# Kernel optimization log

Hardware: AMD Instinct MI355X
Metric: run time of the kernel (lower is better)

The kernel has to match this reference:

```python
import jax, jax.numpy as jnp
import numpy as np

DIM = 1024
NUM_HEADS = 16
HEAD_DIM = DIM // NUM_HEADS
SCALE = HEAD_DIM ** -0.5


def setup_inputs() -> dict:
    key = jax.random.key(0)
    ks = jax.random.split(key, 5)
    B, N, C = 2, 2048, DIM
    x = jax.random.normal(ks[0], (B, N, C), dtype=jnp.float32)
    s = 1.0 / np.sqrt(C)
    W_qkv = jax.random.normal(ks[1], (C, 3 * C), dtype=jnp.float32) * s
    b_qkv = jax.random.normal(ks[2], (3 * C,), dtype=jnp.float32) * 0.01
    W_proj = jax.random.normal(ks[3], (C, C), dtype=jnp.float32) * s
    b_proj = jax.random.normal(ks[4], (C,), dtype=jnp.float32) * 0.01
    return {"x": x, "W_qkv": W_qkv, "b_qkv": b_qkv, "W_proj": W_proj, "b_proj": b_proj}


def reference(x, W_qkv, b_qkv, W_proj, b_proj):
    B, N, C = x.shape
    qkv = x @ W_qkv + b_qkv                      # [B, N, 3C]
    qkv = qkv.reshape(B, N, 3, NUM_HEADS, HEAD_DIM)
    qkv = jnp.transpose(qkv, (2, 0, 3, 1, 4))    # [3, B, H, N, hd]
    # Faithful to source quirk: q = k = v = qkv[2]
    v = qkv[2]
    q = v
    k = v
    attn = jnp.einsum('bhnd,bhmd->bhnm', q, k) * SCALE
    attn = jax.nn.softmax(attn, axis=-1)
    out = jnp.einsum('bhnm,bhmd->bhnd', attn, v)  # [B, H, N, hd]
    out = jnp.transpose(out, (0, 2, 1, 3)).reshape(B, N, C)
    return out @ W_proj + b_proj
```

## Files before the change

### kernel.cpp

```cpp
#include <hip/hip_runtime.h>

typedef __bf16    bf16x4 __attribute__((ext_vector_type(4)));
typedef __bf16    bf16x8 __attribute__((ext_vector_type(8)));
typedef _Float16  f16x2  __attribute__((ext_vector_type(2)));
typedef _Float16  f16x4  __attribute__((ext_vector_type(4)));
typedef _Float16  f16x8  __attribute__((ext_vector_type(8)));
typedef float     f32x4  __attribute__((ext_vector_type(4)));

#define MFMA16x16x32 __builtin_amdgcn_mfma_f32_16x16x32_bf16
#define MFMA16x16x32F __builtin_amdgcn_mfma_f32_16x16x32_f16

__device__ __forceinline__ void gload_lds16(const void* g, void* l) {
  __builtin_amdgcn_global_load_lds((const __attribute__((address_space(1))) void*)g,
                                   (__attribute__((address_space(3))) void*)l, 16, 0, 0);
}

__device__ __forceinline__ f16x2 pkrtz(float a, float b) {
  return __builtin_bit_cast(f16x2, __builtin_amdgcn_cvt_pkrtz(a, b));
}

__global__ __launch_bounds__(256) void prep_all(const float* __restrict__ x,
                                                const float* __restrict__ Wqkv,
                                                const float* __restrict__ Wproj,
                                                __bf16* __restrict__ xb,
                                                __bf16* __restrict__ WvT,
                                                __bf16* __restrict__ WpT) {
  __shared__ float tile[64][65];
  const int t = threadIdx.x;
  if (blockIdx.z == 2) {
    const int bid = blockIdx.x * 16 + blockIdx.y;
#pragma unroll
    for (int c = 0; c < 16; c++) {
      int gid = (bid * 16 + c) * 256 + t;
      float4 v = ((const float4*)x)[gid];
      bf16x4 o;
      o.x = (__bf16)v.x; o.y = (__bf16)v.y; o.z = (__bf16)v.z; o.w = (__bf16)v.w;
      *(bf16x4*)&xb[(size_t)gid * 4] = o;
    }
    return;
  }
  const float* src; __bf16* dst; int ld, c0;
  if (blockIdx.z == 0) { src = Wqkv; dst = WvT; ld = 3072; c0 = 2048; }
  else                 { src = Wproj; dst = WpT; ld = 1024; c0 = 0; }
  const int k0 = blockIdx.x * 64, n0 = blockIdx.y * 64;
#pragma unroll
  for (int i = 0; i < 4; i++) {
    int idx = t + i * 256; int r = idx >> 4, g = idx & 15;
    float4 v = *(const float4*)&src[(size_t)(k0 + r) * ld + c0 + n0 + g * 4];
    tile[r][g * 4 + 0] = v.x; tile[r][g * 4 + 1] = v.y;
    tile[r][g * 4 + 2] = v.z; tile[r][g * 4 + 3] = v.w;
  }
  __syncthreads();
#pragma unroll
  for (int i = 0; i < 4; i++) {
    int idx = t + i * 256; int n = idx >> 4, g = idx & 15;
    bf16x4 o;
    o.x = (__bf16)tile[g * 4 + 0][n]; o.y = (__bf16)tile[g * 4 + 1][n];
    o.z = (__bf16)tile[g * 4 + 2][n]; o.w = (__bf16)tile[g * 4 + 3][n];
    *(bf16x4*)&dst[(size_t)(n0 + n) * 1024 + k0 + g * 4] = o;
  }
}

#define STAGE_TILE(bi, kk)                                            \
  { char* buf_ = (char*)lds + (bi) * 24576;                           \
    const __bf16* a_ = pA + (kk) * 64;                                \
    const __bf16* b_ = pB + (kk) * 64;                                \
    gload_lds16(a_,          buf_ + t * 16);                          \
    gload_lds16(a_ + 32 * K, buf_ + 4096  + t * 16);                  \
    gload_lds16(a_ + 64 * K, buf_ + 8192  + t * 16);                  \
    gload_lds16(a_ + 96 * K, buf_ + 12288 + t * 16);                  \
    gload_lds16(b_,          buf_ + 16384 + t * 16);                  \
    gload_lds16(b_ + 32 * K, buf_ + 20480 + t * 16); }

__global__ __launch_bounds__(256, 2) void gemm_v(const __bf16* __restrict__ xb,
                                                 const __bf16* __restrict__ WvT,
                                                 const float* __restrict__ bias,
                                                 __bf16* __restrict__ V,
                                                 _Float16* __restrict__ Vt) {
  constexpr int K = 1024;
  __shared__ char lds[3 * 24576];
  const int t = threadIdx.x, w = t >> 6, l = t & 63, lr = l & 15, quad = l >> 4;
  const int wr = w >> 1, wc = w & 1;
  const int wgid = blockIdx.x;
  const int xcd = wgid & 7, sub = wgid >> 3;
  const int mb = xcd * 4 + (sub & 3), nb = sub >> 2;
  const int m0 = mb * 128, n0 = nb * 64;

  const int row0 = t >> 3;
  const int scol = (t & 7) ^ (row0 & 7);
  const __bf16* pA = xb  + (size_t)(m0 + row0) * K + scol * 8;
  const __bf16* pB = WvT + (size_t)(n0 + row0) * K + scol * 8;

  f32x4 acc[4][2] = {};
  int aoff[4][2], boff[2][2];
#pragma unroll
  for (int mi = 0; mi < 4; mi++)
#pragma unroll
    for (int ks = 0; ks < 2; ks++)
      aoff[mi][ks] = (wr * 64 + mi * 16 + lr) * 128 + (((ks * 4 + quad) ^ (lr & 7)) * 16);
#pragma unroll
  for (int nc = 0; nc < 2; nc++)
#pragma unroll
    for (int ks = 0; ks < 2; ks++)
      boff[nc][ks] = 16384 + (wc * 32 + nc * 16 + lr) * 128 + (((ks * 4 + quad) ^ (lr & 7)) * 16);

  STAGE_TILE(0, 0);
  STAGE_TILE(1, 1);
  for (int it = 0; it < 16; ++it) {
    if (it < 15) { asm volatile("s_waitcnt vmcnt(6)" ::: "memory"); }
    else         { asm volatile("s_waitcnt vmcnt(0)" ::: "memory"); }
    __builtin_amdgcn_sched_barrier(0);
    __builtin_amdgcn_s_barrier();
    if (it + 2 < 16) STAGE_TILE((it + 2) % 3, it + 2);
    const char* buf = (const char*)lds + (it % 3) * 24576;
    bf16x8 af[4][2], bv[2][2];
#pragma unroll
    for (int mi = 0; mi < 4; mi++)
#pragma unroll
      for (int ks = 0; ks < 2; ks++)
        af[mi][ks] = *(const bf16x8*)(buf + aoff[mi][ks]);
#pragma unroll
    for (int nc = 0; nc < 2; nc++)
#pragma unroll
      for (int ks = 0; ks < 2; ks++)
        bv[nc][ks] = *(const bf16x8*)(buf + boff[nc][ks]);
#pragma unroll
    for (int mi = 0; mi < 4; mi++)
#pragma unroll
      for (int nc = 0; nc < 2; nc++)
#pragma unroll
        for (int ks = 0; ks < 2; ks++)
          acc[mi][nc] = MFMA16x16x32(af[mi][ks], bv[nc][ks], acc[mi][nc], 0, 0, 0);
  }
  __syncthreads();
  char* tbuf = (char*)lds;
#pragma unroll
  for (int mi = 0; mi < 4; mi++) {
    const int grow0 = m0 + wr * 64 + mi * 16 + quad * 4;
    const int tokl = wr * 64 + mi * 16 + quad * 4;
#pragma unroll
    for (int nc = 0; nc < 2; nc++) {
      const int d = wc * 32 + nc * 16 + lr;
      const int gcol = n0 + d;
      float bb = bias[gcol];
      float v0 = acc[mi][nc][0] + bb, v1 = acc[mi][nc][1] + bb;
      float v2 = acc[mi][nc][2] + bb, v3 = acc[mi][nc][3] + bb;
      V[(size_t)(grow0 + 0) * 1024 + gcol] = (__bf16)v0;
      V[(size_t)(grow0 + 1) * 1024 + gcol] = (__bf16)v1;
      V[(size_t)(grow0 + 2) * 1024 + gcol] = (__bf16)v2;
      V[(size_t)(grow0 + 3) * 1024 + gcol] = (__bf16)v3;
      f16x2 lo = pkrtz(v0, v1), hi = pkrtz(v2, v3);
      f16x4 pv; pv[0] = lo[0]; pv[1] = lo[1]; pv[2] = hi[0]; pv[3] = hi[1];
      const int g = (tokl >> 2) ^ ((d & 7) << 2);
      *(f16x4*)(tbuf + d * 256 + g * 8) = pv;
    }
  }
  __syncthreads();
  {
    const int b_ = m0 >> 11, tok0 = m0 & 2047;
    const int d = t >> 2, c = t & 3;
    _Float16* dst = Vt + ((size_t)(b_ * 16 + nb) * 64 + d) * 2048 + tok0 + c * 32;
#pragma unroll
    for (int p2 = 0; p2 < 4; p2++) {
      int g = (c * 8 + p2 * 2) ^ ((d & 7) << 2);
      f16x8 vv = *(const f16x8*)(tbuf + d * 256 + g * 8);
      *(f16x8*)&dst[p2 * 8] = vv;
    }
  }
}

__global__ __launch_bounds__(256, 2) void gemm_proj(const __bf16* __restrict__ A,
                                                    const __bf16* __restrict__ Bt,
                                                    const float* __restrict__ bias,
                                                    float* __restrict__ outp) {
  constexpr int K = 1024, Nn = 1024;
  __shared__ char lds[3 * 24576];
  const int t = threadIdx.x, w = t >> 6, l = t & 63, lr = l & 15, quad = l >> 4;
  const int wr = w >> 1, wc = w & 1;
  const int wgid = blockIdx.x;
  const int xcd = wgid & 7, sub = wgid >> 3;
  const int mb = xcd * 4 + (sub & 3), nb = sub >> 2;
  const int m0 = mb * 128, n0 = nb * 64;

  const int row0 = t >> 3;
  const int scol = (t & 7) ^ (row0 & 7);
  const __bf16* pA = A  + (size_t)(m0 + row0) * K + scol * 8;
  const __bf16* pB = Bt + (size_t)(n0 + row0) * K + scol * 8;

  f32x4 acc[4][2] = {};
  int aoff[4][2], boff[2][2];
#pragma unroll
  for (int mi = 0; mi < 4; mi++)
#pragma unroll
    for (int ks = 0; ks < 2; ks++)
      aoff[mi][ks] = (wr * 64 + mi * 16 + lr) * 128 + (((ks * 4 + quad) ^ (lr & 7)) * 16);
#pragma unroll
  for (int nc = 0; nc < 2; nc++)
#pragma unroll
    for (int ks = 0; ks < 2; ks++)
      boff[nc][ks] = 16384 + (wc * 32 + nc * 16 + lr) * 128 + (((ks * 4 + quad) ^ (lr & 7)) * 16);

  STAGE_TILE(0, 0);
  STAGE_TILE(1, 1);
  for (int it = 0; it < 16; ++it) {
    if (it < 15) { asm volatile("s_waitcnt vmcnt(6)" ::: "memory"); }
    else         { asm volatile("s_waitcnt vmcnt(0)" ::: "memory"); }
    __builtin_amdgcn_sched_barrier(0);
    __builtin_amdgcn_s_barrier();
    if (it + 2 < 16) STAGE_TILE((it + 2) % 3, it + 2);
    const char* buf = (const char*)lds + (it % 3) * 24576;
    bf16x8 af[4][2], bv[2][2];
#pragma unroll
    for (int mi = 0; mi < 4; mi++)
#pragma unroll
      for (int ks = 0; ks < 2; ks++)
        af[mi][ks] = *(const bf16x8*)(buf + aoff[mi][ks]);
#pragma unroll
    for (int nc = 0; nc < 2; nc++)
#pragma unroll
      for (int ks = 0; ks < 2; ks++)
        bv[nc][ks] = *(const bf16x8*)(buf + boff[nc][ks]);
#pragma unroll
    for (int mi = 0; mi < 4; mi++)
#pragma unroll
      for (int nc = 0; nc < 2; nc++)
#pragma unroll
        for (int ks = 0; ks < 2; ks++)
          acc[mi][nc] = MFMA16x16x32(af[mi][ks], bv[nc][ks], acc[mi][nc], 0, 0, 0);
  }
#pragma unroll
  for (int mi = 0; mi < 4; mi++) {
    const int grow0 = m0 + wr * 64 + mi * 16 + quad * 4;
#pragma unroll
    for (int nc = 0; nc < 2; nc++) {
      const int gcol = n0 + wc * 32 + nc * 16 + lr;
      float bb = bias[gcol];
#pragma unroll
      for (int r = 0; r < 4; r++)
        outp[(size_t)(grow0 + r) * Nn + gcol] = acc[mi][nc][r] + bb;
    }
  }
}

__global__ __launch_bounds__(512, 4) void attn_kernel(const __bf16* __restrict__ V,
                                                      const _Float16* __restrict__ Vt,
                                                      __bf16* __restrict__ O) {
  __shared__ char lds[65536];
  const int t = threadIdx.x, w = t >> 6, l = t & 63, lr = l & 15, quad = l >> 4;
  const int bh = blockIdx.x, b = bh >> 4, h = bh & 15;
  const int qb = blockIdx.y * 128 + (w & 3) * 16;
  const int part = w >> 2;

  const __bf16* Vbh = V + (size_t)b * 2048 * 1024 + h * 64;
  const _Float16* Vtbh = Vt + (size_t)bh * 64 * 2048;

  bf16x8 qf[2][2];
#pragma unroll
  for (int sub = 0; sub < 2; sub++)
#pragma unroll
    for (int ks = 0; ks < 2; ks++)
      qf[sub][ks] = *(const bf16x8*)(Vbh + (size_t)(qb + sub * 64 + lr) * 1024 + ks * 32 + quad * 8);

  const int kva = t >> 3, ua = (t & 7) ^ (kva & 7);
  const __bf16* pK0 = Vbh + (size_t)kva * 1024 + ua * 8;
  const __bf16* pK1 = pK0 + (size_t)64 * 1024;
  const int kb_ = t >> 7, d_ = (t >> 1) & 63, qh = (t & 1) ^ ((d_ >> 2) & 1);
  const _Float16* pV0 = Vtbh + (size_t)d_ * 2048 + kb_ * 16 + qh * 8;
  const _Float16* pV1 = pV0 + 64;

  const int koff0 = lr * 128 + ((quad ^ (lr & 7)) * 16);
  const int koff1 = lr * 128 + (((4 + quad) ^ (lr & 7)) * 16);
  const int xq = (quad >> 1) ^ ((lr >> 2) & 1);
  const int voff = lr * 32 + xq * 16 + (quad & 1) * 8;

  f32x4 o[2][4] = {};
  f32x4 l5[2] = {};
  f16x8 ones8;
#pragma unroll
  for (int i = 0; i < 8; i++) ones8[i] = (_Float16)1.0f;
  const float Cc = 0.18033688011112042f;
  const float C8 = 11.541560327111707f;

  {
    char* base = lds;
    gload_lds16(pK0, base + t * 16);
    gload_lds16(pV0, base + 8192 + t * 16);
    gload_lds16(pK1, base + 16384 + t * 16);
    gload_lds16(pV1, base + 24576 + t * 16);
  }
  for (int it = 0; it < 16; ++it) {
    __syncthreads();
    if (it + 1 < 16) {
      pK0 += 131072; pK1 += 131072; pV0 += 128; pV1 += 128;
      char* base = lds + ((it + 1) & 1) * 32768;
      gload_lds16(pK0, base + t * 16);
      gload_lds16(pV0, base + 8192 + t * 16);
      gload_lds16(pK1, base + 16384 + t * 16);
      gload_lds16(pV1, base + 24576 + t * 16);
    }
    const char* Kb = lds + (it & 1) * 32768 + part * 16384;
    const char* Vb = Kb + 8192;

    f32x4 s[2][4] = {};
#pragma unroll
    for (int ks = 0; ks < 2; ks++) {
      const int ko = ks ? koff1 : koff0;
#pragma unroll
      for (int rb = 0; rb < 4; rb++) {
        bf16x8 kf = *(const bf16x8*)(Kb + ko + rb * 2048);
        s[0][rb] = MFMA16x16x32(kf, qf[0][ks], s[0][rb], 0, 0, 0);
        s[1][rb] = MFMA16x16x32(kf, qf[1][ks], s[1][rb], 0, 0, 0);
      }
    }

    f16x8 pf8[2][2];
#pragma unroll
    for (int sub = 0; sub < 2; sub++)
#pragma unroll
      for (int i = 0; i < 2; i++) {
        f16x4 half_[2];
#pragma unroll
        for (int hh = 0; hh < 2; hh++) {
          const int rb = 2 * i + hh;
          float p0 = __builtin_amdgcn_exp2f(s[sub][rb][0] * Cc - C8);
          float p1 = __builtin_amdgcn_exp2f(s[sub][rb][1] * Cc - C8);
          float p2 = __builtin_amdgcn_exp2f(s[sub][rb][2] * Cc - C8);
          float p3 = __builtin_amdgcn_exp2f(s[sub][rb][3] * Cc - C8);
          f16x2 lo = pkrtz(p0, p1);
          f16x2 hi = pkrtz(p2, p3);
          half_[hh][0] = lo[0]; half_[hh][1] = lo[1];
          half_[hh][2] = hi[0]; half_[hh][3] = hi[1];
        }
        pf8[sub][i] = __builtin_shufflevector(half_[0], half_[1], 0, 1, 2, 3, 4, 5, 6, 7);
      }

#pragma unroll
    for (int i = 0; i < 2; i++) {
#pragma unroll
      for (int db = 0; db < 4; db++) {
        f16x4 va = *(const f16x4*)(Vb + voff + db * 512 + (2 * i) * 2048);
        f16x4 vb2 = *(const f16x4*)(Vb + voff + db * 512 + (2 * i + 1) * 2048);
        f16x8 vf8 = __builtin_shufflevector(va, vb2, 0, 1, 2, 3, 4, 5, 6, 7);
        o[0][db] = MFMA16x16x32F(pf8[0][i], vf8, o[0][db], 0, 0, 0);
        o[1][db] = MFMA16x16x32F(pf8[1][i], vf8, o[1][db], 0, 0, 0);
      }
      l5[0] = MFMA16x16x32F(pf8[0][i], ones8, l5[0], 0, 0, 0);
      l5[1] = MFMA16x16x32F(pf8[1][i], ones8, l5[1], 0, 0, 0);
    }
  }

  __syncthreads();
  float* xch = (float*)lds;
  if (w >= 4) {
    float* dsto = xch + (w - 4) * 2048;
#pragma unroll
    for (int sub = 0; sub < 2; sub++)
#pragma unroll
      for (int db = 0; db < 4; db++)
        *(f32x4*)&dsto[(sub * 4 + db) * 256 + l * 4] = o[sub][db];
    float* dstl = xch + 8192 + (w - 4) * 512;
    *(f32x4*)&dstl[l * 4] = l5[0];
    *(f32x4*)&dstl[256 + l * 4] = l5[1];
  }
  __syncthreads();
  if (w < 4) {
    const float* srco = xch + w * 2048;
    const float* srcl = xch + 8192 + w * 512;
#pragma unroll
    for (int sub = 0; sub < 2; sub++) {
#pragma unroll
      for (int db = 0; db < 4; db++)
        o[sub][db] += *(const f32x4*)&srco[(sub * 4 + db) * 256 + l * 4];
      l5[sub] += *(const f32x4*)&srcl[sub * 256 + l * 4];
    }
#pragma unroll
    for (int sub = 0; sub < 2; sub++)
#pragma unroll
      for (int r = 0; r < 4; r++) {
        float lv = 1.0f / l5[sub][r];
        int token = b * 2048 + qb + sub * 64 + quad * 4 + r;
#pragma unroll
        for (int db = 0; db < 4; db++)
          O[(size_t)token * 1024 + h * 64 + db * 16 + lr] = (__bf16)(o[sub][db][r] * lv);
      }
  }
}

extern "C" void kernel_launch(void* const* d_in, const int* in_sizes, int n_in,
                              void* d_out, int out_size, void* d_ws, size_t ws_size,
                              hipStream_t stream) {
  (void)in_sizes; (void)n_in; (void)out_size; (void)ws_size;
  const float* x     = (const float*)d_in[0];
  const float* Wqkv  = (const float*)d_in[1];
  const float* bqkv  = (const float*)d_in[2];
  const float* Wproj = (const float*)d_in[3];
  const float* bproj = (const float*)d_in[4];

  char* ws = (char*)d_ws;
  __bf16*    V   = (__bf16*)(ws);
  _Float16*  Vt  = (_Float16*)(ws + (size_t)8  * 1048576);
  __bf16*    Ob  = (__bf16*)(ws + (size_t)16 * 1048576);
  __bf16*    xb  = (__bf16*)(ws + (size_t)16 * 1048576);
  __bf16*    WvT = (__bf16*)(ws + (size_t)24 * 1048576);
  __bf16*    WpT = (__bf16*)(ws + (size_t)26 * 1048576);

  prep_all<<<dim3(16, 16, 3), 256, 0, stream>>>(x, Wqkv, Wproj, xb, WvT, WpT);
  gemm_v<<<dim3(512), 256, 0, stream>>>(xb, WvT, bqkv + 2048, V, Vt);
  attn_kernel<<<dim3(32, 16), 512, 0, stream>>>(V, Vt, Ob);
  gemm_proj<<<dim3(512), 256, 0, stream>>>(Ob, WpT, bproj, (float*)d_out);
}
```

Measured before the change: 156.8 us.

## Enlarge GEMM tiles to 128x128 with K=32 steps and direct Vt stores

Both GEMMs move from 128x64 output tiles with K=64 stages to 128x128 tiles with K=32 stages, halving the grid to 256 workgroups (one per CU) and raising arithmetic intensity per LDS load. gemm_v also drops the LDS transpose staging for Vt and writes f16x4 strips directly to global memory. The trade-off is lower occupancy (one workgroup per CU), twice as many pipeline iterations with barriers, and less coalesced Vt stores.

```diff
diff --git a/kernel.cpp b/kernel.cpp
--- a/kernel.cpp
+++ b/kernel.cpp
@@ -61,87 +61,72 @@
   }
 }
 
-#define STAGE_TILE(bi, kk)                                            \
-  { char* buf_ = (char*)lds + (bi) * 24576;                           \
-    const __bf16* a_ = pA + (kk) * 64;                                \
-    const __bf16* b_ = pB + (kk) * 64;                                \
+#define STAGE_TILE32(bi, kk)                                          \
+  { char* buf_ = (char*)lds + (bi) * 16384;                           \
+    const __bf16* a_ = pA + (kk) * 32;                                \
+    const __bf16* b_ = pB + (kk) * 32;                                \
     gload_lds16(a_,          buf_ + t * 16);                          \
-    gload_lds16(a_ + 32 * K, buf_ + 4096  + t * 16);                  \
-    gload_lds16(a_ + 64 * K, buf_ + 8192  + t * 16);                  \
-    gload_lds16(a_ + 96 * K, buf_ + 12288 + t * 16);                  \
-    gload_lds16(b_,          buf_ + 16384 + t * 16);                  \
-    gload_lds16(b_ + 32 * K, buf_ + 20480 + t * 16); }
-
-__global__ __launch_bounds__(256, 2) void gemm_v(const __bf16* __restrict__ xb,
+    gload_lds16(a_ + 64 * K, buf_ + 4096  + t * 16);                  \
+    gload_lds16(b_,          buf_ + 8192  + t * 16);                  \
+    gload_lds16(b_ + 64 * K, buf_ + 12288 + t * 16); }
+
+__global__ __launch_bounds__(256, 1) void gemm_v(const __bf16* __restrict__ xb,
                                                  const __bf16* __restrict__ WvT,
                                                  const float* __restrict__ bias,
                                                  __bf16* __restrict__ V,
                                                  _Float16* __restrict__ Vt) {
   constexpr int K = 1024;
-  __shared__ char lds[3 * 24576];
+  __shared__ char lds[3 * 16384];
   const int t = threadIdx.x, w = t >> 6, l = t & 63, lr = l & 15, quad = l >> 4;
   const int wr = w >> 1, wc = w & 1;
   const int wgid = blockIdx.x;
   const int xcd = wgid & 7, sub = wgid >> 3;
   const int mb = xcd * 4 + (sub & 3), nb = sub >> 2;
-  const int m0 = mb * 128, n0 = nb * 64;
-
-  const int row0 = t >> 3;
-  const int scol = (t & 7) ^ (row0 & 7);
+  const int m0 = mb * 128, n0 = nb * 128;
+
+  const int row0 = t >> 2;
+  const int scol = (t & 3) ^ (row0 & 3);
   const __bf16* pA = xb  + (size_t)(m0 + row0) * K + scol * 8;
   const __bf16* pB = WvT + (size_t)(n0 + row0) * K + scol * 8;
 
-  f32x4 acc[4][2] = {};
-  int aoff[4][2], boff[2][2];
+  f32x4 acc[4][4] = {};
+  int aoff[4], boff[4];
 #pragma unroll
   for (int mi = 0; mi < 4; mi++)
-#pragma unroll
-    for (int ks = 0; ks < 2; ks++)
-      aoff[mi][ks] = (wr * 64 + mi * 16 + lr) * 128 + (((ks * 4 + quad) ^ (lr & 7)) * 16);
-#pragma unroll
-  for (int nc = 0; nc < 2; nc++)
-#pragma unroll
-    for (int ks = 0; ks < 2; ks++)
-      boff[nc][ks] = 16384 + (wc * 32 + nc * 16 + lr) * 128 + (((ks * 4 + quad) ^ (lr & 7)) * 16);
-
-  STAGE_TILE(0, 0);
-  STAGE_TILE(1, 1);
-  for (int it = 0; it < 16; ++it) {
-    if (it < 15) { asm volatile("s_waitcnt vmcnt(6)" ::: "memory"); }
+    aoff[mi] = (wr * 64 + mi * 16 + lr) * 64 + ((quad ^ (lr & 3)) * 16);
+#pragma unroll
+  for (int nc = 0; nc < 4; nc++)
+    boff[nc] = 8192 + (wc * 64 + nc * 16 + lr) * 64 + ((quad ^ (lr & 3)) * 16);
+
+  STAGE_TILE32(0, 0);
+  STAGE_TILE32(1, 1);
+  for (int it = 0; it < 32; ++it) {
+    if (it < 31) { asm volatile("s_waitcnt vmcnt(4)" ::: "memory"); }
     else         { asm volatile("s_waitcnt vmcnt(0)" ::: "memory"); }
     __builtin_amdgcn_sched_barrier(0);
     __builtin_amdgcn_s_barrier();
-    if (it + 2 < 16) STAGE_TILE((it + 2) % 3, it + 2);
-    const char* buf = (const char*)lds + (it % 3) * 24576;
-    bf16x8 af[4][2], bv[2][2];
+    if (it + 2 < 32) STAGE_TILE32((it + 2) % 3, it + 2);
+    const char* buf = (const char*)lds + (it % 3) * 16384;
+    bf16x8 af[4], bv[4];
+#pragma unroll
+    for (int mi = 0; mi < 4; mi++) af[mi] = *(const bf16x8*)(buf + aoff[mi]);
+#pragma unroll
+    for (int nc = 0; nc < 4; nc++) bv[nc] = *(const bf16x8*)(buf + boff[nc]);
 #pragma unroll
     for (int mi = 0; mi < 4; mi++)
 #pragma unroll
-      for (int ks = 0; ks < 2; ks++)
-        af[mi][ks] = *(const bf16x8*)(buf + aoff[mi][ks]);
-#pragma unroll
-    for (int nc = 0; nc < 2; nc++)
-#pragma unroll
-      for (int ks = 0; ks < 2; ks++)
-        bv[nc][ks] = *(const bf16x8*)(buf + boff[nc][ks]);
-#pragma unroll
-    for (int mi = 0; mi < 4; mi++)
-#pragma unroll
-      for (int nc = 0; nc < 2; nc++)
-#pragma unroll
-        for (int ks = 0; ks < 2; ks++)
-          acc[mi][nc] = MFMA16x16x32(af[mi][ks], bv[nc][ks], acc[mi][nc], 0, 0, 0);
-  }
-  __syncthreads();
-  char* tbuf = (char*)lds;
+      for (int nc = 0; nc < 4; nc++)
+        acc[mi][nc] = MFMA16x16x32(af[mi], bv[nc], acc[mi][nc], 0, 0, 0);
+  }
+  const int h2 = nb * 2 + wc;
 #pragma unroll
   for (int mi = 0; mi < 4; mi++) {
     const int grow0 = m0 + wr * 64 + mi * 16 + quad * 4;
-    const int tokl = wr * 64 + mi * 16 + quad * 4;
-#pragma unroll
-    for (int nc = 0; nc < 2; nc++) {
-      const int d = wc * 32 + nc * 16 + lr;
-      const int gcol = n0 + d;
+    const int b_ = grow0 >> 11, tok0 = grow0 & 2047;
+#pragma unroll
+    for (int nc = 0; nc < 4; nc++) {
+      const int d2 = nc * 16 + lr;
+      const int gcol = n0 + wc * 64 + d2;
       float bb = bias[gcol];
       float v0 = acc[mi][nc][0] + bb, v1 = acc[mi][nc][1] + bb;
       float v2 = acc[mi][nc][2] + bb, v3 = acc[mi][nc][3] + bb;
@@ -151,89 +136,64 @@
       V[(size_t)(grow0 + 3) * 1024 + gcol] = (__bf16)v3;
       f16x2 lo = pkrtz(v0, v1), hi = pkrtz(v2, v3);
       f16x4 pv; pv[0] = lo[0]; pv[1] = lo[1]; pv[2] = hi[0]; pv[3] = hi[1];
-      const int g = (tokl >> 2) ^ ((d & 7) << 2);
-      *(f16x4*)(tbuf + d * 256 + g * 8) = pv;
-    }
-  }
-  __syncthreads();
-  {
-    const int b_ = m0 >> 11, tok0 = m0 & 2047;
-    const int d = t >> 2, c = t & 3;
-    _Float16* dst = Vt + ((size_t)(b_ * 16 + nb) * 64 + d) * 2048 + tok0 + c * 32;
-#pragma unroll
-    for (int p2 = 0; p2 < 4; p2++) {
-      int g = (c * 8 + p2 * 2) ^ ((d & 7) << 2);
-      f16x8 vv = *(const f16x8*)(tbuf + d * 256 + g * 8);
-      *(f16x8*)&dst[p2 * 8] = vv;
-    }
-  }
-}
-
-__global__ __launch_bounds__(256, 2) void gemm_proj(const __bf16* __restrict__ A,
+      *(f16x4*)&Vt[((size_t)(b_ * 16 + h2) * 64 + d2) * 2048 + tok0] = pv;
+    }
+  }
+}
+
+__global__ __launch_bounds__(256, 1) void gemm_proj(const __bf16* __restrict__ A,
                                                     const __bf16* __restrict__ Bt,
                                                     const float* __restrict__ bias,
                                                     float* __restrict__ outp) {
   constexpr int K = 1024, Nn = 1024;
-  __shared__ char lds[3 * 24576];
+  __shared__ char lds[3 * 16384];
   const int t = threadIdx.x, w = t >> 6, l = t & 63, lr = l & 15, quad = l >> 4;
   const int wr = w >> 1, wc = w & 1;
   const int wgid = blockIdx.x;
   const int xcd = wgid & 7, sub = wgid >> 3;
   const int mb = xcd * 4 + (sub & 3), nb = sub >> 2;
-  const int m0 = mb * 128, n0 = nb * 64;
-
-  const int row0 = t >> 3;
-  const int scol = (t & 7) ^ (row0 & 7);
+  const int m0 = mb * 128, n0 = nb * 128;
+
+  const int row0 = t >> 2;
+  const int scol = (t & 3) ^ (row0 & 3);
   const __bf16* pA = A  + (size_t)(m0 + row0) * K + scol * 8;
   const __bf16* pB = Bt + (size_t)(n0 + row0) * K + scol * 8;
 
-  f32x4 acc[4][2] = {};
-  int aoff[4][2], boff[2][2];
+  f32x4 acc[4][4] = {};
+  int aoff[4], boff[4];
 #pragma unroll
   for (int mi = 0; mi < 4; mi++)
-#pragma unroll
-    for (int ks = 0; ks < 2; ks++)
-      aoff[mi][ks] = (wr * 64 + mi * 16 + lr) * 128 + (((ks * 4 + quad) ^ (lr & 7)) * 16);
-#pragma unroll
-  for (int nc = 0; nc < 2; nc++)
-#pragma unroll
-    for (int ks = 0; ks < 2; ks++)
-      boff[nc][ks] = 16384 + (wc * 32 + nc * 16 + lr) * 128 + (((ks * 4 + quad) ^ (lr & 7)) * 16);
-
-  STAGE_TILE(0, 0);
-  STAGE_TILE(1, 1);
-  for (int it = 0; it < 16; ++it) {
-    if (it < 15) { asm volatile("s_waitcnt vmcnt(6)" ::: "memory"); }
+    aoff[mi] = (wr * 64 + mi * 16 + lr) * 64 + ((quad ^ (lr & 3)) * 16);
+#pragma unroll
+  for (int nc = 0; nc < 4; nc++)
+    boff[nc] = 8192 + (wc * 64 + nc * 16 + lr) * 64 + ((quad ^ (lr & 3)) * 16);
+
+  STAGE_TILE32(0, 0);
+  STAGE_TILE32(1, 1);
+  for (int it = 0; it < 32; ++it) {
+    if (it < 31) { asm volatile("s_waitcnt vmcnt(4)" ::: "memory"); }
     else         { asm volatile("s_waitcnt vmcnt(0)" ::: "memory"); }
     __builtin_amdgcn_sched_barrier(0);
     __builtin_amdgcn_s_barrier();
-    if (it + 2 < 16) STAGE_TILE((it + 2) % 3, it + 2);
-    const char* buf = (const char*)lds + (it % 3) * 24576;
-    bf16x8 af[4][2], bv[2][2];
+    if (it + 2 < 32) STAGE_TILE32((it + 2) % 3, it + 2);
+    const char* buf = (const char*)lds + (it % 3) * 16384;
+    bf16x8 af[4], bv[4];
+#pragma unroll
+    for (int mi = 0; mi < 4; mi++) af[mi] = *(const bf16x8*)(buf + aoff[mi]);
+#pragma unroll
+    for (int nc = 0; nc < 4; nc++) bv[nc] = *(const bf16x8*)(buf + boff[nc]);
 #pragma unroll
     for (int mi = 0; mi < 4; mi++)
 #pragma unroll
-      for (int ks = 0; ks < 2; ks++)
-        af[mi][ks] = *(const bf16x8*)(buf + aoff[mi][ks]);
-#pragma unroll
-    for (int nc = 0; nc < 2; nc++)
-#pragma unroll
-      for (int ks = 0; ks < 2; ks++)
-        bv[nc][ks] = *(const bf16x8*)(buf + boff[nc][ks]);
-#pragma unroll
-    for (int mi = 0; mi < 4; mi++)
-#pragma unroll
-      for (int nc = 0; nc < 2; nc++)
-#pragma unroll
-        for (int ks = 0; ks < 2; ks++)
-          acc[mi][nc] = MFMA16x16x32(af[mi][ks], bv[nc][ks], acc[mi][nc], 0, 0, 0);
+      for (int nc = 0; nc < 4; nc++)
+        acc[mi][nc] = MFMA16x16x32(af[mi], bv[nc], acc[mi][nc], 0, 0, 0);
   }
 #pragma unroll
   for (int mi = 0; mi < 4; mi++) {
     const int grow0 = m0 + wr * 64 + mi * 16 + quad * 4;
 #pragma unroll
-    for (int nc = 0; nc < 2; nc++) {
-      const int gcol = n0 + wc * 32 + nc * 16 + lr;
+    for (int nc = 0; nc < 4; nc++) {
+      const int gcol = n0 + wc * 64 + nc * 16 + lr;
       float bb = bias[gcol];
 #pragma unroll
       for (int r = 0; r < 4; r++)
@@ -405,7 +365,7 @@
   __bf16*    WpT = (__bf16*)(ws + (size_t)26 * 1048576);
 
   prep_all<<<dim3(16, 16, 3), 256, 0, stream>>>(x, Wqkv, Wproj, xb, WvT, WpT);
-  gemm_v<<<dim3(512), 256, 0, stream>>>(xb, WvT, bqkv + 2048, V, Vt);
+  gemm_v<<<dim3(256), 256, 0, stream>>>(xb, WvT, bqkv + 2048, V, Vt);
   attn_kernel<<<dim3(32, 16), 512, 0, stream>>>(V, Vt, Ob);
-  gemm_proj<<<dim3(512), 256, 0, stream>>>(Ob, WpT, bproj, (float*)d_out);
-}
+  gemm_proj<<<dim3(256), 256, 0, stream>>>(Ob, WpT, bproj, (float*)d_out);
+}
```

Result: no change. 157.1 us (+0.2%).
